# Kernel optimization log

Measured on AMD Instinct MI355X. Metric: run time of the kernel, lower is better.

The kernel has to match this reference:

```python
import jax, jax.numpy as jnp
import numpy as np

S, B, F_IN, H = 512, 64, 512, 512  # seq_len, batch, feat_in, feat_out
W_SCALE = 0.04  # keep gates out of saturation, ~ torch default init scale


def setup_inputs() -> dict:
    key = jax.random.key(0)
    k1, k2, k3, k4, k5 = jax.random.split(key, 5)
    return {
        "seq": jax.random.normal(k1, (S, B, F_IN), dtype=jnp.float32),
        "w_ih": jax.random.normal(k2, (4 * H, F_IN), dtype=jnp.float32) * W_SCALE,
        "w_hh": jax.random.normal(k3, (4 * H, H), dtype=jnp.float32) * W_SCALE,
        "b_ih": jax.random.normal(k4, (4 * H,), dtype=jnp.float32) * W_SCALE,
        "b_hh": jax.random.normal(k5, (4 * H,), dtype=jnp.float32) * W_SCALE,
    }


def reference(seq, w_ih, w_hh, b_ih, b_hh):
    # Single-layer LSTM scanned over time; equivalent to the per-timestep
    # nn.LSTM calls in OpenLSTM. PyTorch gate order: i, f, g, o.
    hdim = w_hh.shape[1]
    bias = b_ih + b_hh  # fold biases once

    def step(carry, x):
        h, c = carry
        gates = x @ w_ih.T + h @ w_hh.T + bias  # [B, 4H]
        i, f, g, o = jnp.split(gates, 4, axis=-1)
        c = jax.nn.sigmoid(f) * c + jax.nn.sigmoid(i) * jnp.tanh(g)
        h = jax.nn.sigmoid(o) * jnp.tanh(c)
        return (h, c), (h, c)

    b = seq.shape[1]
    h0 = jnp.zeros((b, hdim), seq.dtype)
    _, (hs, cs) = jax.lax.scan(step, (h0, h0), seq)
    # stack of per-step (h_n, c_n), each with num_layers=1 axis: [S, 1, B, H]
    return hs[:, None, :, :], cs[:, None, :, :]
```

## Files before the change

kernel.cpp:

```cpp
#include <hip/hip_runtime.h>

#define TS 512
#define NB 64
#define FIN 512
#define HD 512
#define HBUF_U64 (NB * HD / 2)
#define R_FAST 16

typedef short bf16x8 __attribute__((ext_vector_type(8)));
typedef float f32x4 __attribute__((ext_vector_type(4)));
typedef unsigned int u32x4 __attribute__((ext_vector_type(4)));

__device__ __forceinline__ unsigned short f2bf(float f) {
  union { float f; unsigned int i; } v; v.f = f;
  unsigned int r = v.i + 0x7fffu + ((v.i >> 16) & 1u);
  return (unsigned short)(r >> 16);
}
__device__ __forceinline__ bf16x8 packv(f32x4 a, f32x4 b) {
  bf16x8 r;
#pragma unroll
  for (int i = 0; i < 4; ++i) r[i] = (short)f2bf(a[i]);
#pragma unroll
  for (int i = 0; i < 4; ++i) r[4 + i] = (short)f2bf(b[i]);
  return r;
}
__device__ __forceinline__ float sigm(float x) { return 1.0f / (1.0f + __expf(-x)); }
__device__ __forceinline__ float tanh_(float x) { return 1.0f - 2.0f / (__expf(2.0f * x) + 1.0f); }

template <int OFF>
__device__ __forceinline__ u32x4 ldx4_dev(const unsigned long long* p) {
  u32x4 v;
  asm volatile("global_load_dwordx4 %0, %1, off offset:%2 sc0 sc1"
               : "=v"(v) : "v"(p), "i"(OFF));
  return v;
}

__global__ void __launch_bounds__(256, 1) lstm_persist(
    const float* __restrict__ seq,
    const float* __restrict__ w_ih,
    const float* __restrict__ w_hh,
    const float* __restrict__ b_ih,
    const float* __restrict__ b_hh,
    float* __restrict__ out,
    unsigned long long* __restrict__ hbuf)
{
  const int wg   = blockIdx.x;
  const int hg   = wg & 63;
  const int bg   = wg >> 6;
  const int tid  = threadIdx.x;
  const int wave = tid >> 6;
  const int lane = tid & 63;
  const int mb0  = bg * 16;
  const int hid0 = hg * 8;
  const int nloc = lane & 15;
  const int quad = lane >> 4;

  __shared__ __align__(16) float gred[2][4][32][20];

  const float* W = (wave < 2) ? w_ih : w_hh;
  const int w   = wave & 1;
  const int k0  = w * 256;

  bf16x8 bfrag[2][8];
#pragma unroll
  for (int nt = 0; nt < 2; ++nt) {
    int n = nt * 16 + nloc;
    int grow = (n >> 3) * HD + hid0 + (n & 7);
    const float* src = W + (size_t)grow * FIN + k0 + quad * 8;
#pragma unroll
    for (int kk = 0; kk < 8; ++kk)
      bfrag[nt][kk] = packv(*(const f32x4*)(src + kk * 32),
                            *(const f32x4*)(src + kk * 32 + 4));
  }

  float bias_[4] = {0.f, 0.f, 0.f, 0.f};
  float cprev = 0.0f;
  int cb = 0, cj = 0;
  if (tid < 128) {
    cb = tid >> 3;
    cj = tid & 7;
#pragma unroll
    for (int g = 0; g < 4; ++g) {
      int r = g * HD + hid0 + cj;
      bias_[g] = b_ih[r] + b_hh[r];
    }
  }

  const size_t ax_base = (size_t)(mb0 + nloc) * FIN + k0 + quad * 8;
  const int rd_base = bg * 4096 + w * 2048 + quad * 64 + nloc * 4;
  const int wr_base = (bg * 64 + hg) * 64;

  f32x4 xpf[16];
  if (wave < 2) {
    const float* ap = seq + ax_base;
#pragma unroll
    for (int kk = 0; kk < 8; ++kk) {
      xpf[2 * kk]     = *(const f32x4*)(ap + kk * 32);
      xpf[2 * kk + 1] = *(const f32x4*)(ap + kk * 32 + 4);
    }
  }

  for (int t = 0; t < TS; ++t) {
    f32x4 acc0 = {0.f, 0.f, 0.f, 0.f};
    f32x4 acc1 = {0.f, 0.f, 0.f, 0.f};

    if (wave < 2) {
      bf16x8 afr[8];
#pragma unroll
      for (int kk = 0; kk < 8; ++kk) afr[kk] = packv(xpf[2 * kk], xpf[2 * kk + 1]);
#pragma unroll
      for (int kk = 0; kk < 8; ++kk) {
        acc0 = __builtin_amdgcn_mfma_f32_16x16x32_bf16(afr[kk], bfrag[0][kk], acc0, 0, 0, 0);
        acc1 = __builtin_amdgcn_mfma_f32_16x16x32_bf16(afr[kk], bfrag[1][kk], acc1, 0, 0, 0);
      }
      int tn = (t + 1 < TS) ? t + 1 : TS - 1;
      const float* ap = seq + (size_t)tn * (NB * FIN) + ax_base;
#pragma unroll
      for (int kk = 0; kk < 8; ++kk) {
        xpf[2 * kk]     = *(const f32x4*)(ap + kk * 32);
        xpf[2 * kk + 1] = *(const f32x4*)(ap + kk * 32 + 4);
      }
    } else if (t > 0) {
      const unsigned long long* hb =
          hbuf + (size_t)((t - 1) & 3) * HBUF_U64 + rd_base;
      unsigned long long hv[32];
      unsigned int pend = 0xffffu;

      for (int r = 0; r < R_FAST && pend; ++r) {
        u32x4 wv[16];
#define ISSUE(p) if (pend & (1u << (p))) \
          wv[p] = ldx4_dev<((((p) >> 1) & 1) * 2048 + ((p) & 1) * 16)>( \
              hb + ((p) >> 2) * 512);
        ISSUE(0)  ISSUE(1)  ISSUE(2)  ISSUE(3)
        ISSUE(4)  ISSUE(5)  ISSUE(6)  ISSUE(7)
        ISSUE(8)  ISSUE(9)  ISSUE(10) ISSUE(11)
        ISSUE(12) ISSUE(13) ISSUE(14) ISSUE(15)
#undef ISSUE
        asm volatile("s_waitcnt vmcnt(0)" ::: "memory");
        __builtin_amdgcn_sched_barrier(0);
#pragma unroll
        for (int p = 0; p < 16; ++p)
          if (pend & (1u << p)) {
            int i0 = (p >> 1) * 4 + (p & 1) * 2;
            unsigned long long a =
                ((unsigned long long)wv[p][1] << 32) | wv[p][0];
            unsigned long long b =
                ((unsigned long long)wv[p][3] << 32) | wv[p][2];
            if ((int)(unsigned int)(a >> 32) >= t &&
                (int)(unsigned int)(b >> 32) >= t) {
              hv[i0] = a; hv[i0 + 1] = b;
              pend &= ~(1u << p);
            }
          }
      }
      if (pend) {
        unsigned int done = 0;
#pragma unroll
        for (int p = 0; p < 16; ++p)
          if (!(pend & (1u << p)))
            done |= 3u << ((p >> 1) * 4 + (p & 1) * 2);
        for (int r = 0; r < 8192 && done != 0xffffffffu; ++r) {
#pragma unroll
          for (int i = 0; i < 32; ++i)
            if (!((done >> i) & 1u))
              hv[i] = __hip_atomic_load(hb + ((i >> 2) * 256 + (i & 3)),
                                        __ATOMIC_RELAXED, __HIP_MEMORY_SCOPE_AGENT);
          unsigned int nd = done;
#pragma unroll
          for (int i = 0; i < 32; ++i)
            if (!((nd >> i) & 1u) && (int)(unsigned int)(hv[i] >> 32) >= t)
              nd |= 1u << i;
          done = nd;
          if (done != 0xffffffffu) __builtin_amdgcn_s_sleep(1);
        }
      }

      bf16x8 afr[8];
#pragma unroll
      for (int kk = 0; kk < 8; ++kk) {
        union { unsigned int d[4]; bf16x8 v; } u;
#pragma unroll
        for (int j = 0; j < 4; ++j) u.d[j] = (unsigned int)hv[kk * 4 + j];
        afr[kk] = u.v;
      }
#pragma unroll
      for (int kk = 0; kk < 8; ++kk) {
        acc0 = __builtin_amdgcn_mfma_f32_16x16x32_bf16(afr[kk], bfrag[0][kk], acc0, 0, 0, 0);
        acc1 = __builtin_amdgcn_mfma_f32_16x16x32_bf16(afr[kk], bfrag[1][kk], acc1, 0, 0, 0);
      }
    }
    *(f32x4*)&gred[t & 1][wave][nloc][quad * 4]      = acc0;
    *(f32x4*)&gred[t & 1][wave][16 + nloc][quad * 4] = acc1;
    __syncthreads();

    if (tid < 128) {
      float gs[4];
#pragma unroll
      for (int g = 0; g < 4; ++g) {
        int n = g * 8 + cj;
        gs[g] = bias_[g] + gred[t & 1][0][n][cb] + gred[t & 1][1][n][cb] +
                gred[t & 1][2][n][cb] + gred[t & 1][3][n][cb];
      }
      float ig = sigm(gs[0]);
      float fg = sigm(gs[1]);
      float gg = tanh_(gs[2]);
      float og = sigm(gs[3]);
      float c  = fg * cprev + ig * gg;
      cprev = c;
      float h  = og * tanh_(c);
      size_t o = (size_t)t * (NB * HD) + (size_t)(mb0 + cb) * HD + hid0 + cj;
      unsigned int hu = (unsigned int)f2bf(h);
      unsigned int ho = __shfl_down(hu, 1);
      if ((tid & 1) == 0) {
        unsigned long long tv =
            ((unsigned long long)(unsigned int)(t + 1) << 32) |
            (unsigned long long)(hu | (ho << 16));
        __hip_atomic_store(hbuf + (size_t)(t & 3) * HBUF_U64 + wr_base +
                               cb * 4 + (cj >> 1), tv,
                           __ATOMIC_RELAXED, __HIP_MEMORY_SCOPE_AGENT);
      }
      out[o] = h;
      out[(size_t)TS * NB * HD + o] = c;
    }
  }
}

extern "C" void kernel_launch(void* const* d_in, const int* in_sizes, int n_in,
                              void* d_out, int out_size, void* d_ws, size_t ws_size,
                              hipStream_t stream) {
  const float* seq = (const float*)d_in[0];
  const float* wih = (const float*)d_in[1];
  const float* whh = (const float*)d_in[2];
  const float* bih = (const float*)d_in[3];
  const float* bhh = (const float*)d_in[4];
  float* out = (float*)d_out;
  unsigned long long* hbuf = (unsigned long long*)d_ws;
  hipLaunchKernelGGL(lstm_persist, dim3(256), dim3(256), 0, stream,
                     seq, wih, whh, bih, bhh, out, hbuf);
}
```

Before: 2.262 ms.

## Use 128 workgroups of 512 threads, each owning 16 hidden units

```diff
diff --git a/kernel.cpp b/kernel.cpp
--- a/kernel.cpp
+++ b/kernel.cpp
@@ -35,7 +35,7 @@
   return v;
 }
 
-__global__ void __launch_bounds__(256, 1) lstm_persist(
+__global__ void __launch_bounds__(512, 1) lstm_persist(
     const float* __restrict__ seq,
     const float* __restrict__ w_ih,
     const float* __restrict__ w_hh,
@@ -45,27 +45,28 @@
     unsigned long long* __restrict__ hbuf)
 {
   const int wg   = blockIdx.x;
-  const int hg   = wg & 63;
-  const int bg   = wg >> 6;
+  const int bg   = wg & 3;
+  const int hg   = wg >> 2;
   const int tid  = threadIdx.x;
-  const int wave = tid >> 6;
+  const int w    = tid >> 6;
   const int lane = tid & 63;
+  const int m    = w >> 2;
+  const int kh   = (w >> 1) & 1;
+  const int ch   = w & 1;
   const int mb0  = bg * 16;
-  const int hid0 = hg * 8;
+  const int hid0 = hg * 16;
   const int nloc = lane & 15;
   const int quad = lane >> 4;
-
-  __shared__ __align__(16) float gred[2][4][32][20];
-
-  const float* W = (wave < 2) ? w_ih : w_hh;
-  const int w   = wave & 1;
-  const int k0  = w * 256;
+  const int k0   = kh * 256;
+
+  __shared__ __align__(16) float gred[2][8][32][20];
+
+  const float* W = (m == 0) ? w_ih : w_hh;
 
   bf16x8 bfrag[2][8];
 #pragma unroll
   for (int nt = 0; nt < 2; ++nt) {
-    int n = nt * 16 + nloc;
-    int grow = (n >> 3) * HD + hid0 + (n & 7);
+    int grow = (ch * 2 + nt) * HD + hid0 + nloc;
     const float* src = W + (size_t)grow * FIN + k0 + quad * 8;
 #pragma unroll
     for (int kk = 0; kk < 8; ++kk)
@@ -76,9 +77,9 @@
   float bias_[4] = {0.f, 0.f, 0.f, 0.f};
   float cprev = 0.0f;
   int cb = 0, cj = 0;
-  if (tid < 128) {
-    cb = tid >> 3;
-    cj = tid & 7;
+  if (tid < 256) {
+    cb = tid >> 4;
+    cj = tid & 15;
 #pragma unroll
     for (int g = 0; g < 4; ++g) {
       int r = g * HD + hid0 + cj;
@@ -87,11 +88,12 @@
   }
 
   const size_t ax_base = (size_t)(mb0 + nloc) * FIN + k0 + quad * 8;
-  const int rd_base = bg * 4096 + w * 2048 + quad * 64 + nloc * 4;
-  const int wr_base = (bg * 64 + hg) * 64;
+  const int rd_base = bg * 4096 + kh * 2048 + (quad >> 1) * 128 + nloc * 8 +
+                      (quad & 1) * 4;
+  const int wr_base = (bg * 32 + hg) * 128;
 
   f32x4 xpf[16];
-  if (wave < 2) {
+  if (m == 0) {
     const float* ap = seq + ax_base;
 #pragma unroll
     for (int kk = 0; kk < 8; ++kk) {
@@ -104,7 +106,7 @@
     f32x4 acc0 = {0.f, 0.f, 0.f, 0.f};
     f32x4 acc1 = {0.f, 0.f, 0.f, 0.f};
 
-    if (wave < 2) {
+    if (m == 0) {
       bf16x8 afr[8];
 #pragma unroll
       for (int kk = 0; kk < 8; ++kk) afr[kk] = packv(xpf[2 * kk], xpf[2 * kk + 1]);
@@ -129,8 +131,7 @@
       for (int r = 0; r < R_FAST && pend; ++r) {
         u32x4 wv[16];
 #define ISSUE(p) if (pend & (1u << (p))) \
-          wv[p] = ldx4_dev<((((p) >> 1) & 1) * 2048 + ((p) & 1) * 16)>( \
-              hb + ((p) >> 2) * 512);
+          wv[p] = ldx4_dev<(((p) & 1) * 16)>(hb + ((p) >> 1) * 256);
         ISSUE(0)  ISSUE(1)  ISSUE(2)  ISSUE(3)
         ISSUE(4)  ISSUE(5)  ISSUE(6)  ISSUE(7)
         ISSUE(8)  ISSUE(9)  ISSUE(10) ISSUE(11)
@@ -189,17 +190,18 @@
         acc1 = __builtin_amdgcn_mfma_f32_16x16x32_bf16(afr[kk], bfrag[1][kk], acc1, 0, 0, 0);
       }
     }
-    *(f32x4*)&gred[t & 1][wave][nloc][quad * 4]      = acc0;
-    *(f32x4*)&gred[t & 1][wave][16 + nloc][quad * 4] = acc1;
+    *(f32x4*)&gred[t & 1][w][nloc][quad * 4]      = acc0;
+    *(f32x4*)&gred[t & 1][w][16 + nloc][quad * 4] = acc1;
     __syncthreads();
 
-    if (tid < 128) {
+    if (tid < 256) {
       float gs[4];
 #pragma unroll
       for (int g = 0; g < 4; ++g) {
-        int n = g * 8 + cj;
-        gs[g] = bias_[g] + gred[t & 1][0][n][cb] + gred[t & 1][1][n][cb] +
-                gred[t & 1][2][n][cb] + gred[t & 1][3][n][cb];
+        int wv0 = g >> 1;
+        int n   = (g & 1) * 16 + cj;
+        gs[g] = bias_[g] + gred[t & 1][wv0][n][cb] + gred[t & 1][wv0 + 2][n][cb] +
+                gred[t & 1][wv0 + 4][n][cb] + gred[t & 1][wv0 + 6][n][cb];
       }
       float ig = sigm(gs[0]);
       float fg = sigm(gs[1]);
@@ -216,7 +218,7 @@
             ((unsigned long long)(unsigned int)(t + 1) << 32) |
             (unsigned long long)(hu | (ho << 16));
         __hip_atomic_store(hbuf + (size_t)(t & 3) * HBUF_U64 + wr_base +
-                               cb * 4 + (cj >> 1), tv,
+                               cb * 8 + (cj >> 1), tv,
                            __ATOMIC_RELAXED, __HIP_MEMORY_SCOPE_AGENT);
       }
       out[o] = h;
@@ -235,6 +237,6 @@
   const float* bhh = (const float*)d_in[4];
   float* out = (float*)d_out;
   unsigned long long* hbuf = (unsigned long long*)d_ws;
-  hipLaunchKernelGGL(lstm_persist, dim3(256), dim3(256), 0, stream,
+  hipLaunchKernelGGL(lstm_persist, dim3(128), dim3(512), 0, stream,
                      seq, wih, whh, bih, bhh, out, hbuf);
 }
```

Result: slower. 3.813 ms (+68.5%).
